# Optimization experiments

Measured on AMD Instinct MI355X. Metric: run time of the kernel, lower is better.

Reference implementation:

```python
import jax, jax.numpy as jnp
import numpy as np

D = 512
O = 64

def setup_inputs() -> dict:
    key = jax.random.key(0)
    k1, k2, k3, k4 = jax.random.split(key, 4)
    B, N, F, V = 4, 1024, 16, 64
    x = jax.random.normal(k1, (B, N, D), dtype=jnp.float32)
    idx = jax.random.randint(k2, (B, F), 0, V)
    feature_bias_table = jax.random.normal(k3, (V, D), dtype=jnp.float32)
    out_projection_table = jax.random.normal(k4, (V, D * O), dtype=jnp.float32) * (1.0 / np.sqrt(D))
    return {"x": x, "idx": idx, "feature_bias_table": feature_bias_table,
            "out_projection_table": out_projection_table}

def reference(x, idx, feature_bias_table, out_projection_table):
    # x: [B,N,D], idx: [B,F]
    w = out_projection_table[idx].reshape(*idx.shape, D, O)   # [B,F,D,O]
    b = feature_bias_table[idx]                               # [B,F,D]
    xb = x[:, :, None, :] + b[:, None, :, :]                  # [B,N,F,D]
    out = jnp.einsum('bnfd,bfdo->bnfo', xb, w)                # [B,N,F,O]
    return out
```

## Files before the change

kernel.cpp:

```cpp
#include <hip/hip_runtime.h>
#include <hip/hip_bf16.h>
#include <stdint.h>


typedef __bf16 bf16_t;
typedef __bf16 bf16x8 __attribute__((ext_vector_type(8)));
typedef float floatx4 __attribute__((ext_vector_type(4)));

__device__ __forceinline__ void async_ld16(const bf16_t* g, bf16_t* l) {
    __builtin_amdgcn_global_load_lds(
        (const __attribute__((address_space(1))) void*)g,
        (__attribute__((address_space(3))) void*)l,
        16, 0, 0);
}

__global__ __launch_bounds__(256) void prep_kernel(
    const float* __restrict__ w,
    const float* __restrict__ bias,
    const float* __restrict__ x,
    bf16_t* __restrict__ wt,
    float* __restrict__ cv,
    bf16_t* __restrict__ xb)
{
    const int t = threadIdx.x;
    if (blockIdx.x >= 64) {
        const int base = (blockIdx.x - 64) * 2048 + t * 8;
        const float4 f0 = *(const float4*)(x + base);
        const float4 f1 = *(const float4*)(x + base + 4);
        bf16x8 o;
        o[0] = (bf16_t)f0.x; o[1] = (bf16_t)f0.y;
        o[2] = (bf16_t)f0.z; o[3] = (bf16_t)f0.w;
        o[4] = (bf16_t)f1.x; o[5] = (bf16_t)f1.y;
        o[6] = (bf16_t)f1.z; o[7] = (bf16_t)f1.w;
        *(bf16x8*)(xb + base) = o;
        return;
    }

    const int v = blockIdx.x;
    __shared__ float tile[64][68];
    __shared__ float bch[64];
    __shared__ float red[4][64];

    const int r  = t >> 2, cs = (t & 3) * 16;
    const int o  = t >> 2, ds = (t & 3) * 16;
    const int dq = t >> 6, oc = t & 63;
    float csum = 0.f;
    const float* wv = w + (size_t)v * 32768;

    float4 rg0, rg1, rg2, rg3;
    {
        const float* src = wv + (size_t)r * 64 + cs;
        rg0 = *(const float4*)(src);
        rg1 = *(const float4*)(src + 4);
        rg2 = *(const float4*)(src + 8);
        rg3 = *(const float4*)(src + 12);
    }
    for (int c = 0; c < 8; ++c) {
        __syncthreads();
        *(float4*)&tile[r][cs]      = rg0;
        *(float4*)&tile[r][cs + 4]  = rg1;
        *(float4*)&tile[r][cs + 8]  = rg2;
        *(float4*)&tile[r][cs + 12] = rg3;
        if (t < 64) bch[t] = bias[v * 512 + c * 64 + t];
        __syncthreads();
        if (c < 7) {
            const float* src = wv + (size_t)((c + 1) * 64 + r) * 64 + cs;
            rg0 = *(const float4*)(src);
            rg1 = *(const float4*)(src + 4);
            rg2 = *(const float4*)(src + 8);
            rg3 = *(const float4*)(src + 12);
        }
        bf16x8 t0, t1;
#pragma unroll
        for (int j = 0; j < 8; ++j) t0[j] = (bf16_t)tile[ds + j][o];
#pragma unroll
        for (int j = 0; j < 8; ++j) t1[j] = (bf16_t)tile[ds + 8 + j][o];
        bf16_t* dst = wt + ((size_t)v * 64 + o) * 512 + c * 64 + ds;
        *(bf16x8*)&dst[0] = t0;
        *(bf16x8*)&dst[8] = t1;
#pragma unroll
        for (int j = 0; j < 16; ++j) {
            const int dl = dq * 16 + j;
            csum += bch[dl] * tile[dl][oc];
        }
    }
    red[dq][oc] = csum;
    __syncthreads();
    if (t < 64) cv[v * 64 + t] = red[0][t] + red[1][t] + red[2][t] + red[3][t];
}

__global__ __launch_bounds__(256, 3) void gemm_kernel(
    const bf16_t* __restrict__ xb,
    const bf16_t* __restrict__ wt,
    const float*  __restrict__ cv,
    const int*    __restrict__ idx,
    float* __restrict__ out)
{
    const int bid = blockIdx.x;
    const int f  = bid >> 5;
    const int b  = (bid >> 3) & 3;
    const int mt = bid & 7;
    const int v  = idx[b * 16 + f];

    const int tid  = threadIdx.x;
    const int lane = tid & 63;
    const int wave = tid >> 6;
    const int wm = wave >> 1;
    const int wn = wave & 1;
    const int l15 = lane & 15;
    const int l4  = lane >> 4;

    const bf16_t* Ag = xb + (size_t)(b * 1024 + mt * 128) * 512;
    const bf16_t* Bg = wt + (size_t)v * 64 * 512;

    __shared__ __align__(16) bf16_t As[2][128 * 64];
    __shared__ __align__(16) bf16_t Bs[2][64 * 64];

    floatx4 acc[4][2] = {};

    int a_row[4], a_col[4];
#pragma unroll
    for (int j = 0; j < 4; ++j) {
        const int s = tid + 256 * j;
        a_row[j] = s >> 3;
        a_col[j] = ((s & 7) ^ (a_row[j] & 7)) * 8;
    }
    int b_row[2], b_col[2];
#pragma unroll
    for (int j = 0; j < 2; ++j) {
        const int s = tid + 256 * j;
        b_row[j] = s >> 3;
        b_col[j] = ((s & 7) ^ (b_row[j] & 7)) * 8;
    }

#pragma unroll
    for (int j = 0; j < 4; ++j)
        async_ld16(Ag + a_row[j] * 512 + a_col[j], &As[0][(tid + 256 * j) * 8]);
#pragma unroll
    for (int j = 0; j < 2; ++j)
        async_ld16(Bg + b_row[j] * 512 + b_col[j], &Bs[0][(tid + 256 * j) * 8]);

    for (int kk = 0; kk < 8; ++kk) {
        const int buf = kk & 1;
        __syncthreads();
        if (kk < 7) {
            const int k0 = (kk + 1) * 64;
#pragma unroll
            for (int j = 0; j < 4; ++j)
                async_ld16(Ag + a_row[j] * 512 + k0 + a_col[j],
                           &As[buf ^ 1][(tid + 256 * j) * 8]);
#pragma unroll
            for (int j = 0; j < 2; ++j)
                async_ld16(Bg + b_row[j] * 512 + k0 + b_col[j],
                           &Bs[buf ^ 1][(tid + 256 * j) * 8]);
        }
        bf16x8 a[4][2], bb[2][2];
#pragma unroll
        for (int mi = 0; mi < 4; ++mi) {
            const int row = wm * 64 + mi * 16 + l15;
#pragma unroll
            for (int ks = 0; ks < 2; ++ks)
                a[mi][ks] = *(const bf16x8*)
                    &As[buf][row * 64 + (((ks * 4 + l4) ^ (row & 7)) * 8)];
        }
#pragma unroll
        for (int ni = 0; ni < 2; ++ni) {
            const int row = wn * 32 + ni * 16 + l15;
#pragma unroll
            for (int ks = 0; ks < 2; ++ks)
                bb[ni][ks] = *(const bf16x8*)
                    &Bs[buf][row * 64 + (((ks * 4 + l4) ^ (row & 7)) * 8)];
        }
#pragma unroll
        for (int mi = 0; mi < 4; ++mi)
#pragma unroll
            for (int ni = 0; ni < 2; ++ni) {
                acc[mi][ni] = __builtin_amdgcn_mfma_f32_16x16x32_bf16(
                    a[mi][0], bb[ni][0], acc[mi][ni], 0, 0, 0);
                acc[mi][ni] = __builtin_amdgcn_mfma_f32_16x16x32_bf16(
                    a[mi][1], bb[ni][1], acc[mi][ni], 0, 0, 0);
            }
    }

    const int colbase = wn * 32 + l15;
    const float c0 = cv[v * 64 + colbase];
    const float c1 = cv[v * 64 + colbase + 16];
    float* outp = out + (size_t)(b * 1024 + mt * 128 + wm * 64 + l4 * 4) * 1024
                      + f * 64;
#pragma unroll
    for (int mi = 0; mi < 4; ++mi) {
#pragma unroll
        for (int r = 0; r < 4; ++r) {
            float* row = outp + (size_t)(mi * 16 + r) * 1024;
            row[colbase]      = acc[mi][0][r] + c0;
            row[colbase + 16] = acc[mi][1][r] + c1;
        }
    }
}

__global__ __launch_bounds__(256) void naive_kernel(
    const float* __restrict__ x, const float* __restrict__ w,
    const float* __restrict__ bias, const int* __restrict__ idx,
    float* __restrict__ out)
{
    const int b = blockIdx.x >> 10;
    const int n = blockIdx.x & 1023;
    __shared__ float xr[512];
    for (int d = threadIdx.x; d < 512; d += 256)
        xr[d] = x[(size_t)(b * 1024 + n) * 512 + d];
    __syncthreads();
    for (int p = threadIdx.x; p < 1024; p += 256) {
        const int f = p >> 6, o = p & 63;
        const int v = idx[b * 16 + f];
        const float* wp = w + (size_t)v * 32768 + o;
        const float* bp = bias + v * 512;
        float s = 0.f;
        for (int d = 0; d < 512; ++d)
            s += (xr[d] + bp[d]) * wp[(size_t)d * 64];
        out[(size_t)(b * 1024 + n) * 1024 + p] = s;
    }
}

extern "C" void kernel_launch(void* const* d_in, const int* in_sizes, int n_in,
                              void* d_out, int out_size, void* d_ws, size_t ws_size,
                              hipStream_t stream) {
    const float* x    = (const float*)d_in[0];
    const int*   idx  = (const int*)d_in[1];
    const float* bias = (const float*)d_in[2];
    const float* w    = (const float*)d_in[3];
    float* out = (float*)d_out;

    const size_t cv_bytes = 64 * 64 * sizeof(float);
    const size_t wt_bytes = (size_t)64 * 64 * 512 * 2;
    const size_t xb_bytes = (size_t)4096 * 512 * 2;
    if (ws_size >= cv_bytes + wt_bytes + xb_bytes) {
        float*  cv = (float*)d_ws;
        bf16_t* wt = (bf16_t*)((char*)d_ws + cv_bytes);
        bf16_t* xb = (bf16_t*)((char*)d_ws + cv_bytes + wt_bytes);
        prep_kernel<<<1088, 256, 0, stream>>>(w, bias, x, wt, cv, xb);
        gemm_kernel<<<512, 256, 0, stream>>>(xb, wt, cv, idx, out);
    } else {
        naive_kernel<<<4096, 256, 0, stream>>>(x, w, bias, idx, out);
    }
}
```

Before: 89.96 us.

## Split weight prep across chunks with atomics and load B operand directly to registers

The prep kernel now gives each (vocab, k-chunk) pair its own block instead of looping over 8 chunks per vocab entry. This raises the transpose stage from 64 to 512 blocks, and the bias-projection partial sums are combined with atomicAdd after a memset of cv. The GEMM drops the B shared-memory tiles and loads B fragments straight from global memory into double-buffered registers, with the occupancy hint lowered from 3 to 2. The intent is to fill more of the GPU during prep and to cut LDS traffic and barriers for B. In exchange it adds an extra memset launch, makes the float sums order-nondeterministic, and raises register pressure.

```diff
diff --git a/kernel.cpp b/kernel.cpp
--- a/kernel.cpp
+++ b/kernel.cpp
@@ -23,8 +23,8 @@
     bf16_t* __restrict__ xb)
 {
     const int t = threadIdx.x;
-    if (blockIdx.x >= 64) {
-        const int base = (blockIdx.x - 64) * 2048 + t * 8;
+    if (blockIdx.x >= 512) {
+        const int base = (blockIdx.x - 512) * 2048 + t * 8;
         const float4 f0 = *(const float4*)(x + base);
         const float4 f1 = *(const float4*)(x + base + 4);
         bf16x8 o;
@@ -36,60 +36,45 @@
         return;
     }
 
-    const int v = blockIdx.x;
+    const int v = blockIdx.x >> 3;
+    const int c = blockIdx.x & 7;
     __shared__ float tile[64][68];
     __shared__ float bch[64];
     __shared__ float red[4][64];
 
-    const int r  = t >> 2, cs = (t & 3) * 16;
-    const int o  = t >> 2, ds = (t & 3) * 16;
+    const int r = t >> 2, cs = (t & 3) * 16;
+    const float* src = w + (size_t)v * 32768 + (size_t)(c * 64 + r) * 64 + cs;
+    *(float4*)&tile[r][cs]      = *(const float4*)(src);
+    *(float4*)&tile[r][cs + 4]  = *(const float4*)(src + 4);
+    *(float4*)&tile[r][cs + 8]  = *(const float4*)(src + 8);
+    *(float4*)&tile[r][cs + 12] = *(const float4*)(src + 12);
+    if (t < 64) bch[t] = bias[v * 512 + c * 64 + t];
+    __syncthreads();
+
+    const int o = t >> 2, ds = (t & 3) * 16;
+    bf16x8 t0, t1;
+#pragma unroll
+    for (int j = 0; j < 8; ++j) t0[j] = (bf16_t)tile[ds + j][o];
+#pragma unroll
+    for (int j = 0; j < 8; ++j) t1[j] = (bf16_t)tile[ds + 8 + j][o];
+    bf16_t* dst = wt + ((size_t)v * 64 + o) * 512 + c * 64 + ds;
+    *(bf16x8*)&dst[0] = t0;
+    *(bf16x8*)&dst[8] = t1;
+
     const int dq = t >> 6, oc = t & 63;
     float csum = 0.f;
-    const float* wv = w + (size_t)v * 32768;
-
-    float4 rg0, rg1, rg2, rg3;
-    {
-        const float* src = wv + (size_t)r * 64 + cs;
-        rg0 = *(const float4*)(src);
-        rg1 = *(const float4*)(src + 4);
-        rg2 = *(const float4*)(src + 8);
-        rg3 = *(const float4*)(src + 12);
-    }
-    for (int c = 0; c < 8; ++c) {
-        __syncthreads();
-        *(float4*)&tile[r][cs]      = rg0;
-        *(float4*)&tile[r][cs + 4]  = rg1;
-        *(float4*)&tile[r][cs + 8]  = rg2;
-        *(float4*)&tile[r][cs + 12] = rg3;
-        if (t < 64) bch[t] = bias[v * 512 + c * 64 + t];
-        __syncthreads();
-        if (c < 7) {
-            const float* src = wv + (size_t)((c + 1) * 64 + r) * 64 + cs;
-            rg0 = *(const float4*)(src);
-            rg1 = *(const float4*)(src + 4);
-            rg2 = *(const float4*)(src + 8);
-            rg3 = *(const float4*)(src + 12);
-        }
-        bf16x8 t0, t1;
-#pragma unroll
-        for (int j = 0; j < 8; ++j) t0[j] = (bf16_t)tile[ds + j][o];
-#pragma unroll
-        for (int j = 0; j < 8; ++j) t1[j] = (bf16_t)tile[ds + 8 + j][o];
-        bf16_t* dst = wt + ((size_t)v * 64 + o) * 512 + c * 64 + ds;
-        *(bf16x8*)&dst[0] = t0;
-        *(bf16x8*)&dst[8] = t1;
-#pragma unroll
-        for (int j = 0; j < 16; ++j) {
-            const int dl = dq * 16 + j;
-            csum += bch[dl] * tile[dl][oc];
-        }
+#pragma unroll
+    for (int j = 0; j < 16; ++j) {
+        const int dl = dq * 16 + j;
+        csum += bch[dl] * tile[dl][oc];
     }
     red[dq][oc] = csum;
     __syncthreads();
-    if (t < 64) cv[v * 64 + t] = red[0][t] + red[1][t] + red[2][t] + red[3][t];
-}
-
-__global__ __launch_bounds__(256, 3) void gemm_kernel(
+    if (t < 64) atomicAdd(&cv[v * 64 + t],
+                          red[0][t] + red[1][t] + red[2][t] + red[3][t]);
+}
+
+__global__ __launch_bounds__(256, 2) void gemm_kernel(
     const bf16_t* __restrict__ xb,
     const bf16_t* __restrict__ wt,
     const float*  __restrict__ cv,
@@ -114,7 +99,6 @@
     const bf16_t* Bg = wt + (size_t)v * 64 * 512;
 
     __shared__ __align__(16) bf16_t As[2][128 * 64];
-    __shared__ __align__(16) bf16_t Bs[2][64 * 64];
 
     floatx4 acc[4][2] = {};
 
@@ -125,20 +109,21 @@
         a_row[j] = s >> 3;
         a_col[j] = ((s & 7) ^ (a_row[j] & 7)) * 8;
     }
-    int b_row[2], b_col[2];
-#pragma unroll
-    for (int j = 0; j < 2; ++j) {
-        const int s = tid + 256 * j;
-        b_row[j] = s >> 3;
-        b_col[j] = ((s & 7) ^ (b_row[j] & 7)) * 8;
-    }
+
+    const bf16_t* bp[2];
+#pragma unroll
+    for (int ni = 0; ni < 2; ++ni)
+        bp[ni] = Bg + (size_t)(wn * 32 + ni * 16 + l15) * 512 + l4 * 8;
 
 #pragma unroll
     for (int j = 0; j < 4; ++j)
         async_ld16(Ag + a_row[j] * 512 + a_col[j], &As[0][(tid + 256 * j) * 8]);
-#pragma unroll
-    for (int j = 0; j < 2; ++j)
-        async_ld16(Bg + b_row[j] * 512 + b_col[j], &Bs[0][(tid + 256 * j) * 8]);
+    bf16x8 breg[2][2][2];
+#pragma unroll
+    for (int ni = 0; ni < 2; ++ni)
+#pragma unroll
+        for (int ks = 0; ks < 2; ++ks)
+            breg[0][ni][ks] = *(const bf16x8*)(bp[ni] + ks * 32);
 
     for (int kk = 0; kk < 8; ++kk) {
         const int buf = kk & 1;
@@ -150,11 +135,13 @@
                 async_ld16(Ag + a_row[j] * 512 + k0 + a_col[j],
                            &As[buf ^ 1][(tid + 256 * j) * 8]);
 #pragma unroll
-            for (int j = 0; j < 2; ++j)
-                async_ld16(Bg + b_row[j] * 512 + k0 + b_col[j],
-                           &Bs[buf ^ 1][(tid + 256 * j) * 8]);
+            for (int ni = 0; ni < 2; ++ni)
+#pragma unroll
+                for (int ks = 0; ks < 2; ++ks)
+                    breg[buf ^ 1][ni][ks] =
+                        *(const bf16x8*)(bp[ni] + k0 + ks * 32);
         }
-        bf16x8 a[4][2], bb[2][2];
+        bf16x8 a[4][2];
 #pragma unroll
         for (int mi = 0; mi < 4; ++mi) {
             const int row = wm * 64 + mi * 16 + l15;
@@ -164,21 +151,13 @@
                     &As[buf][row * 64 + (((ks * 4 + l4) ^ (row & 7)) * 8)];
         }
 #pragma unroll
-        for (int ni = 0; ni < 2; ++ni) {
-            const int row = wn * 32 + ni * 16 + l15;
-#pragma unroll
-            for (int ks = 0; ks < 2; ++ks)
-                bb[ni][ks] = *(const bf16x8*)
-                    &Bs[buf][row * 64 + (((ks * 4 + l4) ^ (row & 7)) * 8)];
-        }
-#pragma unroll
         for (int mi = 0; mi < 4; ++mi)
 #pragma unroll
             for (int ni = 0; ni < 2; ++ni) {
                 acc[mi][ni] = __builtin_amdgcn_mfma_f32_16x16x32_bf16(
-                    a[mi][0], bb[ni][0], acc[mi][ni], 0, 0, 0);
+                    a[mi][0], breg[buf][ni][0], acc[mi][ni], 0, 0, 0);
                 acc[mi][ni] = __builtin_amdgcn_mfma_f32_16x16x32_bf16(
-                    a[mi][1], bb[ni][1], acc[mi][ni], 0, 0, 0);
+                    a[mi][1], breg[buf][ni][1], acc[mi][ni], 0, 0, 0);
             }
     }
 
@@ -237,7 +216,8 @@
         float*  cv = (float*)d_ws;
         bf16_t* wt = (bf16_t*)((char*)d_ws + cv_bytes);
         bf16_t* xb = (bf16_t*)((char*)d_ws + cv_bytes + wt_bytes);
-        prep_kernel<<<1088, 256, 0, stream>>>(w, bias, x, wt, cv, xb);
+        hipMemsetAsync(cv, 0, cv_bytes, stream);
+        prep_kernel<<<1536, 256, 0, stream>>>(w, bias, x, wt, cv, xb);
         gemm_kernel<<<512, 256, 0, stream>>>(xb, wt, cv, idx, out);
     } else {
         naive_kernel<<<4096, 256, 0, stream>>>(x, w, bias, idx, out);
```

Measured after the change: 91.24 us. Within noise of the previous version (+1.4%).
